# Kernel optimization log

Measured on AMD Instinct MI355X. Metric: run time of the kernel, lower is better.

Reference implementation:

```python
import jax, jax.numpy as jnp
import numpy as np
from jax import lax

EPS = 1e-5
TEM = 10.0  # self.tem at init; tem_proportion buffer is 0 so it stays 10.0


def _conv1d(x, w, padding, dilation=1, groups=1):
    # x: [B, C, S], w: [O, I//groups, K]
    return lax.conv_general_dilated(
        x, w, window_strides=(1,), padding=[(padding, padding)],
        rhs_dilation=(dilation,), dimension_numbers=('NCH', 'OIH', 'NCH'),
        feature_group_count=groups)


def _bn(y, gamma, beta):
    # training-mode BatchNorm1d: stats over (batch, length) per channel
    m = y.mean(axis=(0, 2), keepdims=True)
    v = y.var(axis=(0, 2), keepdims=True)
    return (y - m) * lax.rsqrt(v + EPS) * gamma[None, :, None] + beta[None, :, None]


def _nor_conv(x, w, g, b, k):
    return _bn(_conv1d(jax.nn.relu(x), w, padding=k // 2), g, b)


def _dil_conv(x, wd, wp, g, b, k):
    C = x.shape[1]
    y = _conv1d(jax.nn.relu(x), wd, padding=k - 1, dilation=2, groups=C)
    y = _conv1d(y, wp, padding=0)
    return _bn(y, g, b)


def _avg_pool3(x):
    s = lax.reduce_window(x, 0.0, lax.add, (1, 1, 3), (1, 1, 1),
                          [(0, 0), (0, 0), (1, 1)])
    return s / 3.0  # count_include_pad=True


def _max_pool3(x):
    return lax.reduce_window(x, -jnp.inf, lax.max, (1, 1, 3), (1, 1, 1),
                             [(0, 0), (0, 0), (1, 1)])


def _forward(x, u, arch_parameters,
             w_nor3, g_nor3, b_nor3, w_nor5, g_nor5, b_nor5,
             w_nor7, g_nor7, b_nor7,
             wd_dil3, wp_dil3, g_dil3, b_dil3,
             wd_dil5, wp_dil5, g_dil5, b_dil5,
             wd_dil7, wp_dil7, g_dil7, b_dil7):
    # ---- Gumbel straight-through gate (get_gumbel_prob) ----
    uc = jnp.clip(u, 1e-9, 1.0 - 1e-9)
    gumbels = -jnp.log(-jnp.log(uc))  # -log(Exp(1) sample)
    logits = (jax.nn.log_softmax(arch_parameters, axis=1) + gumbels) / TEM
    probs = jax.nn.softmax(logits, axis=1)          # [1, 10]
    index = jnp.argmax(probs, axis=-1)              # [1]
    one_h = jax.nn.one_hot(index, probs.shape[-1], dtype=probs.dtype)
    hardwts = one_h - lax.stop_gradient(probs) + probs  # straight-through

    # ---- forward_gdas: single edge (max_nodes=2) ----
    xc = jnp.transpose(x, (0, 2, 1))  # [B, H, S]: hidden=channels, seq=length
    branches = [
        lambda t: jnp.zeros_like(t),                         # none
        _avg_pool3,                                          # avg_pool_3
        _max_pool3,                                          # max_pool_3
        lambda t: _nor_conv(t, w_nor3, g_nor3, b_nor3, 3),   # nor_conv_3
        lambda t: _nor_conv(t, w_nor5, g_nor5, b_nor5, 5),   # nor_conv_5
        lambda t: _nor_conv(t, w_nor7, g_nor7, b_nor7, 7),   # nor_conv_7
        lambda t: _dil_conv(t, wd_dil3, wp_dil3, g_dil3, b_dil3, 3),
        lambda t: _dil_conv(t, wd_dil5, wp_dil5, g_dil5, b_dil5, 5),
        lambda t: _dil_conv(t, wd_dil7, wp_dil7, g_dil7, b_dil7, 7),
        lambda t: t,                                         # skip_connect
    ]
    idx = index[0]
    w = hardwts[0]                                  # [10]
    sel = lax.switch(idx, branches, xc)             # only argmax op is run
    w_sel = jnp.take(w, idx)
    # GDAS: w[argmax]*op(x) + sum of remaining scalar weights (broadcast add)
    out = w_sel * sel + (jnp.sum(w) - w_sel)
    out = jnp.transpose(out, (0, 2, 1))             # back to [B, S, H]
    return out + x                                  # residual


def setup_inputs() -> dict:
    key = jax.random.key(0)
    ks = jax.random.split(key, 16)
    B, S, H = 8, 512, 768
    d = {
        'x': jax.random.normal(ks[0], (B, S, H), jnp.float32),
        'u': jax.random.uniform(ks[1], (1, 10), jnp.float32),
        'arch_parameters': 0.001 * jax.random.normal(ks[2], (1, 10), jnp.float32),
    }
    i = 3
    for k in (3, 5, 7):
        d[f'w_nor{k}'] = 0.02 * jax.random.normal(ks[i], (H, H, k), jnp.float32); i += 1
        d[f'g_nor{k}'] = jnp.ones((H,), jnp.float32)
        d[f'b_nor{k}'] = jnp.zeros((H,), jnp.float32)
    for k in (3, 5, 7):
        d[f'wd_dil{k}'] = 0.1 * jax.random.normal(ks[i], (H, 1, k), jnp.float32); i += 1
        d[f'wp_dil{k}'] = 0.02 * jax.random.normal(ks[i], (H, H, 1), jnp.float32); i += 1
        d[f'g_dil{k}'] = jnp.ones((H,), jnp.float32)
        d[f'b_dil{k}'] = jnp.zeros((H,), jnp.float32)
    return d


def reference(x, u, arch_parameters,
              w_nor3, g_nor3, b_nor3, w_nor5, g_nor5, b_nor5,
              w_nor7, g_nor7, b_nor7,
              wd_dil3, wp_dil3, g_dil3, b_dil3,
              wd_dil5, wp_dil5, g_dil5, b_dil5,
              wd_dil7, wp_dil7, g_dil7, b_dil7):
    return _forward(x, u, arch_parameters,
                    w_nor3, g_nor3, b_nor3, w_nor5, g_nor5, b_nor5,
                    w_nor7, g_nor7, b_nor7,
                    wd_dil3, wp_dil3, g_dil3, b_dil3,
                    wd_dil5, wp_dil5, g_dil5, b_dil5,
                    wd_dil7, wp_dil7, g_dil7, b_dil7)
```

## Files before the change

### kernel.cpp

```cpp
#include <hip/hip_runtime.h>
#include <math.h>

#define BB 8
#define SS 512
#define HH 768
#define NTOT (BB*SS*HH)
#define EPSBN 1e-5f

typedef __attribute__((ext_vector_type(8))) short short8v;
typedef __attribute__((ext_vector_type(4))) float float4v;

struct Params {
  const float *x, *u, *ap;
  const float *w_nor3, *g_nor3, *b_nor3;
  const float *w_nor5, *g_nor5, *b_nor5;
  const float *w_nor7, *g_nor7, *b_nor7;
  const float *wd3, *wp3, *gd3, *bd3;
  const float *wd5, *wp5, *gd5, *bd5;
  const float *wd7, *wp7, *gd7, *bd7;
  float *out;
  float *hdr;
  float *y;
  float *z;
  float *psum;
  float *psq;
  float *mbuf;
  float *ibuf;
};

__device__ __forceinline__ short f2bf(float f) {
  union { float f; unsigned u; } v; v.f = f;
  unsigned r = v.u + 0x7FFF + ((v.u >> 16) & 1);
  return (short)(r >> 16);
}

__global__ void gate_kernel(Params p) {
  if (threadIdx.x != 0 || blockIdx.x != 0) return;
  float ap[10], lg[10], pr[10];
  float mx = -INFINITY;
  for (int i = 0; i < 10; i++) { ap[i] = p.ap[i]; mx = fmaxf(mx, ap[i]); }
  float se = 0.f;
  for (int i = 0; i < 10; i++) se += expf(ap[i] - mx);
  float lse = mx + logf(se);
  float lmax = -INFINITY;
  for (int i = 0; i < 10; i++) {
    float uc = fminf(fmaxf(p.u[i], 1e-9f), 1.f - 1e-9f);
    float gb = -logf(-logf(uc));
    lg[i] = ((ap[i] - lse) + gb) * 0.1f;
    lmax = fmaxf(lmax, lg[i]);
  }
  float ps = 0.f;
  for (int i = 0; i < 10; i++) { pr[i] = expf(lg[i] - lmax); ps += pr[i]; }
  int idx = 0; float best = -INFINITY;
  for (int i = 0; i < 10; i++) {
    pr[i] /= ps;
    if (pr[i] > best) { best = pr[i]; idx = i; }
  }
  float w_sel = (1.0f - pr[idx]) + pr[idx];
  p.hdr[0] = w_sel;
  p.hdr[1] = 0.0f;
  ((int*)p.hdr)[2] = idx;
}

__global__ __launch_bounds__(256) void dw_kernel(Params p) {
  int idx = ((const int*)p.hdr)[2];
  if (idx < 6 || idx > 8) return;
  int k = 3 + 2 * (idx - 6);
  const float* wd = (idx == 6) ? p.wd3 : (idx == 7) ? p.wd5 : p.wd7;
  int tid = blockIdx.x * 256 + threadIdx.x;
  if (tid >= NTOT) return;
  int c = tid % HH;
  int bs = tid / HH;
  int s = bs % SS;
  int b = bs / SS;
  float acc = 0.f;
  for (int dk = 0; dk < k; dk++) {
    int ss = s + 2 * dk - (k - 1);
    if (ss >= 0 && ss < SS) {
      float v = p.x[((size_t)(b * SS + ss)) * HH + c];
      acc += fmaxf(v, 0.f) * wd[c * k + dk];
    }
  }
  p.z[tid] = acc;
}

#define BM 128
#define BN 64
#define BK 32
#define LROW 40
__global__ __launch_bounds__(256) void conv_gemm_kernel(Params p) {
  int idx = ((const int*)p.hdr)[2];
  if (idx < 3 || idx > 8) return;
  bool nor = (idx <= 5);
  int k = nor ? (3 + 2 * (idx - 3)) : (3 + 2 * (idx - 6));
  const float* W = nor ? ((idx == 3) ? p.w_nor3 : (idx == 4) ? p.w_nor5 : p.w_nor7)
                       : ((idx == 6) ? p.wp3 : (idx == 7) ? p.wp5 : p.wp7);
  const float* A = nor ? p.x : p.z;
  int taps = nor ? k : 1;
  int halo = nor ? (k >> 1) : 0;

  __shared__ __attribute__((aligned(16))) short As[BM * LROW];
  __shared__ __attribute__((aligned(16))) short Bs[BN * LROW];

  int mt = blockIdx.x;
  int b = mt >> 2;
  int s0 = (mt & 3) * BM;
  int o0 = blockIdx.y * BN;

  int t = threadIdx.x;
  int lane = t & 63;
  int wid = t >> 6;
  int wm0 = (wid >> 1) * 64;
  int wn0 = (wid & 1) * 32;
  int l16 = lane & 15;
  int quad = lane >> 4;

  int sa_m = t >> 1;
  int sa_h = t & 1;
  int sb_n = t >> 2;
  int sb_seg = t & 3;

  float4v acc[4][2];
#pragma unroll
  for (int mi = 0; mi < 4; mi++)
#pragma unroll
    for (int ni = 0; ni < 2; ni++) acc[mi][ni] = (float4v){0.f, 0.f, 0.f, 0.f};

  for (int dk = 0; dk < taps; dk++) {
    int shift = dk - halo;
    for (int k0 = 0; k0 < HH; k0 += BK) {
      {
        int srow = s0 + sa_m + shift;
        float4 f[4];
        if (srow >= 0 && srow < SS) {
          const float* ap = A + ((size_t)(b * SS + srow)) * HH + k0 + sa_h * 16;
#pragma unroll
          for (int j = 0; j < 4; j++) f[j] = ((const float4*)ap)[j];
        } else {
#pragma unroll
          for (int j = 0; j < 4; j++) f[j] = (float4){0.f, 0.f, 0.f, 0.f};
        }
        short h16[16];
#pragma unroll
        for (int j = 0; j < 4; j++) {
          float vx = f[j].x, vy = f[j].y, vz = f[j].z, vw = f[j].w;
          if (nor) { vx = fmaxf(vx, 0.f); vy = fmaxf(vy, 0.f); vz = fmaxf(vz, 0.f); vw = fmaxf(vw, 0.f); }
          h16[4 * j + 0] = f2bf(vx); h16[4 * j + 1] = f2bf(vy);
          h16[4 * j + 2] = f2bf(vz); h16[4 * j + 3] = f2bf(vw);
        }
        short* dst = &As[sa_m * LROW + sa_h * 16];
        *(short8v*)dst = *(short8v*)&h16[0];
        *(short8v*)(dst + 8) = *(short8v*)&h16[8];
      }
      {
        short h8[8];
        int o = o0 + sb_n;
        if (!nor) {
          const float* bp = W + (size_t)o * HH + k0 + sb_seg * 8;
          float4 f0 = ((const float4*)bp)[0];
          float4 f1 = ((const float4*)bp)[1];
          h8[0] = f2bf(f0.x); h8[1] = f2bf(f0.y); h8[2] = f2bf(f0.z); h8[3] = f2bf(f0.w);
          h8[4] = f2bf(f1.x); h8[5] = f2bf(f1.y); h8[6] = f2bf(f1.z); h8[7] = f2bf(f1.w);
        } else {
#pragma unroll
          for (int j = 0; j < 8; j++) {
            int i = k0 + sb_seg * 8 + j;
            h8[j] = f2bf(W[((size_t)o * HH + i) * k + dk]);
          }
        }
        *(short8v*)&Bs[sb_n * LROW + sb_seg * 8] = *(short8v*)&h8[0];
      }
      __syncthreads();

      short8v af[4], bf[2];
#pragma unroll
      for (int mi = 0; mi < 4; mi++)
        af[mi] = *(const short8v*)&As[(wm0 + mi * 16 + l16) * LROW + quad * 8];
#pragma unroll
      for (int ni = 0; ni < 2; ni++)
        bf[ni] = *(const short8v*)&Bs[(wn0 + ni * 16 + l16) * LROW + quad * 8];
#pragma unroll
      for (int mi = 0; mi < 4; mi++)
#pragma unroll
        for (int ni = 0; ni < 2; ni++)
          acc[mi][ni] = __builtin_amdgcn_mfma_f32_16x16x32_bf16(af[mi], bf[ni], acc[mi][ni], 0, 0, 0);
      __syncthreads();
    }
  }

#pragma unroll
  for (int mi = 0; mi < 4; mi++) {
#pragma unroll
    for (int ni = 0; ni < 2; ni++) {
      int col = o0 + wn0 + ni * 16 + l16;
#pragma unroll
      for (int r = 0; r < 4; r++) {
        int row = s0 + wm0 + mi * 16 + quad * 4 + r;
        p.y[((size_t)(b * SS + row)) * HH + col] = acc[mi][ni][r];
      }
    }
  }
}

__global__ __launch_bounds__(256) void bn_stats1(Params p) {
  int idx = ((const int*)p.hdr)[2];
  if (idx < 3 || idx > 8) return;
  int t = threadIdx.x;
  int c = blockIdx.y * 64 + (t & 63);
  int rsub = t >> 6;
  float s = 0.f, q = 0.f;
  int rbase = blockIdx.x * 256 + rsub;
  for (int j = 0; j < 64; j++) {
    float v = p.y[(size_t)(rbase + 4 * j) * HH + c];
    s += v; q += v * v;
  }
  __shared__ float red[2][4][64];
  red[0][rsub][t & 63] = s;
  red[1][rsub][t & 63] = q;
  __syncthreads();
  if (t < 64) {
    float ts = red[0][0][t] + red[0][1][t] + red[0][2][t] + red[0][3][t];
    float tq = red[1][0][t] + red[1][1][t] + red[1][2][t] + red[1][3][t];
    p.psum[blockIdx.x * HH + blockIdx.y * 64 + t] = ts;
    p.psq[blockIdx.x * HH + blockIdx.y * 64 + t] = tq;
  }
}

__global__ __launch_bounds__(256) void bn_stats2(Params p) {
  int idx = ((const int*)p.hdr)[2];
  if (idx < 3 || idx > 8) return;
  int c = blockIdx.x * 256 + threadIdx.x;
  if (c >= HH) return;
  float s = 0.f, q = 0.f;
  for (int j = 0; j < 16; j++) { s += p.psum[j * HH + c]; q += p.psq[j * HH + c]; }
  float mean = s * (1.f / 4096.f);
  float var = q * (1.f / 4096.f) - mean * mean;
  p.mbuf[c] = mean;
  p.ibuf[c] = rsqrtf(var + EPSBN);
}

__global__ __launch_bounds__(256) void epilogue_kernel(Params p) {
  int idx = ((const int*)p.hdr)[2];
  float w_sel = p.hdr[0], w_rest = p.hdr[1];
  int tid = blockIdx.x * 256 + threadIdx.x;
  if (tid >= NTOT) return;
  float xv = p.x[tid];
  float sel;
  if (idx >= 3 && idx <= 8) {
    const float* g = (idx == 3) ? p.g_nor3 : (idx == 4) ? p.g_nor5 : (idx == 5) ? p.g_nor7
                   : (idx == 6) ? p.gd3 : (idx == 7) ? p.gd5 : p.gd7;
    const float* be = (idx == 3) ? p.b_nor3 : (idx == 4) ? p.b_nor5 : (idx == 5) ? p.b_nor7
                    : (idx == 6) ? p.bd3 : (idx == 7) ? p.bd5 : p.bd7;
    int h = tid % HH;
    float yv = p.y[tid];
    sel = (yv - p.mbuf[h]) * p.ibuf[h] * g[h] + be[h];
  } else if (idx == 0) {
    sel = 0.f;
  } else if (idx == 9) {
    sel = xv;
  } else {
    int bs = tid / HH;
    int s = bs % SS;
    if (idx == 1) {
      float xm = (s > 0) ? p.x[tid - HH] : 0.f;
      float xp = (s < SS - 1) ? p.x[tid + HH] : 0.f;
      sel = (xm + xv + xp) * (1.f / 3.f);
    } else {
      float xm = (s > 0) ? p.x[tid - HH] : -INFINITY;
      float xp = (s < SS - 1) ? p.x[tid + HH] : -INFINITY;
      sel = fmaxf(fmaxf(xm, xv), xp);
    }
  }
  p.out[tid] = w_sel * sel + w_rest + xv;
}

extern "C" void kernel_launch(void* const* d_in, const int* in_sizes, int n_in,
                              void* d_out, int out_size, void* d_ws, size_t ws_size,
                              hipStream_t stream) {
  Params p;
  p.x = (const float*)d_in[0];
  p.u = (const float*)d_in[1];
  p.ap = (const float*)d_in[2];
  p.w_nor3 = (const float*)d_in[3];  p.g_nor3 = (const float*)d_in[4];  p.b_nor3 = (const float*)d_in[5];
  p.w_nor5 = (const float*)d_in[6];  p.g_nor5 = (const float*)d_in[7];  p.b_nor5 = (const float*)d_in[8];
  p.w_nor7 = (const float*)d_in[9];  p.g_nor7 = (const float*)d_in[10]; p.b_nor7 = (const float*)d_in[11];
  p.wd3 = (const float*)d_in[12]; p.wp3 = (const float*)d_in[13]; p.gd3 = (const float*)d_in[14]; p.bd3 = (const float*)d_in[15];
  p.wd5 = (const float*)d_in[16]; p.wp5 = (const float*)d_in[17]; p.gd5 = (const float*)d_in[18]; p.bd5 = (const float*)d_in[19];
  p.wd7 = (const float*)d_in[20]; p.wp7 = (const float*)d_in[21]; p.gd7 = (const float*)d_in[22]; p.bd7 = (const float*)d_in[23];
  p.out = (float*)d_out;

  char* ws = (char*)d_ws;
  size_t off = 0;
  p.hdr = (float*)(ws + off); off += 256;
  p.y   = (float*)(ws + off); off += (size_t)NTOT * 4;
  p.z   = (float*)(ws + off); off += (size_t)NTOT * 4;
  p.psum = (float*)(ws + off); off += 16 * HH * 4;
  p.psq  = (float*)(ws + off); off += 16 * HH * 4;
  p.mbuf = (float*)(ws + off); off += HH * 4;
  p.ibuf = (float*)(ws + off); off += HH * 4;

  int nblk = (NTOT + 255) / 256;

  hipLaunchKernelGGL(gate_kernel, dim3(1), dim3(64), 0, stream, p);
  hipLaunchKernelGGL(dw_kernel, dim3(nblk), dim3(256), 0, stream, p);
  hipLaunchKernelGGL(conv_gemm_kernel, dim3(32, HH / BN), dim3(256), 0, stream, p);
  hipLaunchKernelGGL(bn_stats1, dim3(16, HH / 64), dim3(256), 0, stream, p);
  hipLaunchKernelGGL(bn_stats2, dim3((HH + 255) / 256), dim3(256), 0, stream, p);
  hipLaunchKernelGGL(epilogue_kernel, dim3(nblk), dim3(256), 0, stream, p);
}
```

Measured before the change: 145.1 us.

## Pre-convert activations and weights to bf16, use direct-to-LDS loads, fuse BN stats

```diff
diff --git a/kernel.cpp b/kernel.cpp
--- a/kernel.cpp
+++ b/kernel.cpp
@@ -6,6 +6,8 @@
 #define HH 768
 #define NTOT (BB*SS*HH)
 #define EPSBN 1e-5f
+#define SPAD 4
+#define SROWS (SS + 2*SPAD)
 
 typedef __attribute__((ext_vector_type(8))) short short8v;
 typedef __attribute__((ext_vector_type(4))) float float4v;
@@ -21,11 +23,10 @@
   float *out;
   float *hdr;
   float *y;
-  float *z;
+  short *xb;
+  short *wb;
   float *psum;
   float *psq;
-  float *mbuf;
-  float *ibuf;
 };
 
 __device__ __forceinline__ short f2bf(float f) {
@@ -35,7 +36,9 @@
 }
 
 __global__ void gate_kernel(Params p) {
-  if (threadIdx.x != 0 || blockIdx.x != 0) return;
+  int t = threadIdx.x;
+  for (int i = t; i < HH; i += 64) { p.psum[i] = 0.f; p.psq[i] = 0.f; }
+  if (t != 0) return;
   float ap[10], lg[10], pr[10];
   float mx = -INFINITY;
   for (int i = 0; i < 10; i++) { ap[i] = p.ap[i]; mx = fmaxf(mx, ap[i]); }
@@ -62,45 +65,96 @@
   ((int*)p.hdr)[2] = idx;
 }
 
-__global__ __launch_bounds__(256) void dw_kernel(Params p) {
+#define XBLK 1560
+#define WBLK 2016
+__global__ __launch_bounds__(256) void prep_kernel(Params p) {
   int idx = ((const int*)p.hdr)[2];
-  if (idx < 6 || idx > 8) return;
-  int k = 3 + 2 * (idx - 6);
-  const float* wd = (idx == 6) ? p.wd3 : (idx == 7) ? p.wd5 : p.wd7;
-  int tid = blockIdx.x * 256 + threadIdx.x;
-  if (tid >= NTOT) return;
-  int c = tid % HH;
-  int bs = tid / HH;
-  int s = bs % SS;
-  int b = bs / SS;
-  float acc = 0.f;
-  for (int dk = 0; dk < k; dk++) {
-    int ss = s + 2 * dk - (k - 1);
-    if (ss >= 0 && ss < SS) {
-      float v = p.x[((size_t)(b * SS + ss)) * HH + c];
-      acc += fmaxf(v, 0.f) * wd[c * k + dk];
-    }
-  }
-  p.z[tid] = acc;
+  if (idx < 3 || idx > 8) return;
+  int t = threadIdx.x;
+  if (blockIdx.x < XBLK) {
+    int u = blockIdx.x * 256 + t;
+    int c0 = (u % 96) * 8;
+    int row = (u / 96) % SROWS;
+    int b = u / (96 * SROWS);
+    int s = row - SPAD;
+    short8v o8 = (short8v){0,0,0,0,0,0,0,0};
+    if (s >= 0 && s < SS) {
+      float v[8];
+      if (idx <= 5) {
+        const float* xp = p.x + ((size_t)(b * SS + s) * HH + c0);
+        float4 f0 = ((const float4*)xp)[0];
+        float4 f1 = ((const float4*)xp)[1];
+        v[0] = fmaxf(f0.x, 0.f); v[1] = fmaxf(f0.y, 0.f);
+        v[2] = fmaxf(f0.z, 0.f); v[3] = fmaxf(f0.w, 0.f);
+        v[4] = fmaxf(f1.x, 0.f); v[5] = fmaxf(f1.y, 0.f);
+        v[6] = fmaxf(f1.z, 0.f); v[7] = fmaxf(f1.w, 0.f);
+      } else {
+        int k = 3 + 2 * (idx - 6);
+        const float* wd = (idx == 6) ? p.wd3 : (idx == 7) ? p.wd5 : p.wd7;
+#pragma unroll
+        for (int j = 0; j < 8; j++) v[j] = 0.f;
+        for (int dk = 0; dk < k; dk++) {
+          int ss = s + 2 * dk - (k - 1);
+          if (ss < 0 || ss >= SS) continue;
+          const float* xp = p.x + ((size_t)(b * SS + ss) * HH + c0);
+          float4 f0 = ((const float4*)xp)[0];
+          float4 f1 = ((const float4*)xp)[1];
+          float ff[8] = {f0.x, f0.y, f0.z, f0.w, f1.x, f1.y, f1.z, f1.w};
+#pragma unroll
+          for (int j = 0; j < 8; j++)
+            v[j] += fmaxf(ff[j], 0.f) * wd[(c0 + j) * k + dk];
+        }
+      }
+#pragma unroll
+      for (int j = 0; j < 8; j++) o8[j] = f2bf(v[j]);
+    }
+    *(short8v*)(p.xb + (size_t)(b * SROWS + row) * HH + c0) = o8;
+  } else {
+    int u = (blockIdx.x - XBLK) * 256 + t;
+    int i0 = (u % 96) * 8;
+    int o = (u / 96) % HH;
+    int dk = u / (96 * HH);
+    short8v o8;
+    if (idx <= 5) {
+      int k = 3 + 2 * (idx - 3);
+      if (dk >= k) return;
+      const float* W = (idx == 3) ? p.w_nor3 : (idx == 4) ? p.w_nor5 : p.w_nor7;
+#pragma unroll
+      for (int j = 0; j < 8; j++)
+        o8[j] = f2bf(W[((size_t)o * HH + i0 + j) * k + dk]);
+      *(short8v*)(p.wb + ((size_t)dk * HH + o) * HH + i0) = o8;
+    } else {
+      if (dk != 0) return;
+      const float* W = (idx == 6) ? p.wp3 : (idx == 7) ? p.wp5 : p.wp7;
+      const float* wp0 = W + (size_t)o * HH + i0;
+      float4 f0 = ((const float4*)wp0)[0];
+      float4 f1 = ((const float4*)wp0)[1];
+      o8[0] = f2bf(f0.x); o8[1] = f2bf(f0.y); o8[2] = f2bf(f0.z); o8[3] = f2bf(f0.w);
+      o8[4] = f2bf(f1.x); o8[5] = f2bf(f1.y); o8[6] = f2bf(f1.z); o8[7] = f2bf(f1.w);
+      *(short8v*)(p.wb + (size_t)o * HH + i0) = o8;
+    }
+  }
 }
 
 #define BM 128
 #define BN 64
-#define BK 32
-#define LROW 40
+#define BK 64
+
+typedef const __attribute__((address_space(1))) unsigned int* gas_t;
+typedef __attribute__((address_space(3))) unsigned int* las_t;
+__device__ __forceinline__ void gload16(const void* g, void* l) {
+  __builtin_amdgcn_global_load_lds((gas_t)g, (las_t)l, 16, 0, 0);
+}
+
 __global__ __launch_bounds__(256) void conv_gemm_kernel(Params p) {
   int idx = ((const int*)p.hdr)[2];
   if (idx < 3 || idx > 8) return;
   bool nor = (idx <= 5);
-  int k = nor ? (3 + 2 * (idx - 3)) : (3 + 2 * (idx - 6));
-  const float* W = nor ? ((idx == 3) ? p.w_nor3 : (idx == 4) ? p.w_nor5 : p.w_nor7)
-                       : ((idx == 6) ? p.wp3 : (idx == 7) ? p.wp5 : p.wp7);
-  const float* A = nor ? p.x : p.z;
-  int taps = nor ? k : 1;
-  int halo = nor ? (k >> 1) : 0;
-
-  __shared__ __attribute__((aligned(16))) short As[BM * LROW];
-  __shared__ __attribute__((aligned(16))) short Bs[BN * LROW];
+  int taps = nor ? (3 + 2 * (idx - 3)) : 1;
+  int halo = nor ? (taps >> 1) : 0;
+
+  __shared__ __attribute__((aligned(16))) short As[BM * BK];
+  __shared__ __attribute__((aligned(16))) short Bs[BN * BK];
 
   int mt = blockIdx.x;
   int b = mt >> 2;
@@ -109,87 +163,77 @@
 
   int t = threadIdx.x;
   int lane = t & 63;
-  int wid = t >> 6;
-  int wm0 = (wid >> 1) * 64;
-  int wn0 = (wid & 1) * 32;
-  int l16 = lane & 15;
-  int quad = lane >> 4;
-
-  int sa_m = t >> 1;
-  int sa_h = t & 1;
-  int sb_n = t >> 2;
-  int sb_seg = t & 3;
+  int w = t >> 6;
+  int l16 = lane & 15, quad = lane >> 4;
+  int wm0 = (w >> 1) * 64;
+  int wn0 = (w & 1) * 32;
+  int lr = lane >> 3;
+  int sw8 = ((lane & 7) ^ lr) * 8;
+
+  short* Al0 = &As[(32 * w) * BK];
+  short* Bl0 = &Bs[(16 * w) * BK];
 
   float4v acc[4][2];
 #pragma unroll
   for (int mi = 0; mi < 4; mi++)
 #pragma unroll
     for (int ni = 0; ni < 2; ni++) acc[mi][ni] = (float4v){0.f, 0.f, 0.f, 0.f};
+
+  const char* Ac = (const char*)As;
+  const char* Bc = (const char*)Bs;
+  int aro[4], bro[2], co[2];
+#pragma unroll
+  for (int mi = 0; mi < 4; mi++) aro[mi] = (wm0 + mi * 16 + l16) * (BK * 2);
+#pragma unroll
+  for (int ni = 0; ni < 2; ni++) bro[ni] = (wn0 + ni * 16 + l16) * (BK * 2);
+  int sx = (l16 & 7) << 4;
+  co[0] = (quad * 16) ^ sx;
+  co[1] = (64 + quad * 16) ^ sx;
 
   for (int dk = 0; dk < taps; dk++) {
     int shift = dk - halo;
+    const short* Ag[4]; const short* Bg[2];
+#pragma unroll
+    for (int j = 0; j < 4; j++) {
+      int tr = 32 * w + 8 * j + lr;
+      Ag[j] = p.xb + (size_t)(b * SROWS + SPAD + s0 + shift + tr) * HH + sw8;
+    }
+#pragma unroll
+    for (int j = 0; j < 2; j++) {
+      int tr = 16 * w + 8 * j + lr;
+      Bg[j] = p.wb + ((size_t)dk * HH + o0 + tr) * HH + sw8;
+    }
     for (int k0 = 0; k0 < HH; k0 += BK) {
-      {
-        int srow = s0 + sa_m + shift;
-        float4 f[4];
-        if (srow >= 0 && srow < SS) {
-          const float* ap = A + ((size_t)(b * SS + srow)) * HH + k0 + sa_h * 16;
-#pragma unroll
-          for (int j = 0; j < 4; j++) f[j] = ((const float4*)ap)[j];
-        } else {
-#pragma unroll
-          for (int j = 0; j < 4; j++) f[j] = (float4){0.f, 0.f, 0.f, 0.f};
-        }
-        short h16[16];
-#pragma unroll
-        for (int j = 0; j < 4; j++) {
-          float vx = f[j].x, vy = f[j].y, vz = f[j].z, vw = f[j].w;
-          if (nor) { vx = fmaxf(vx, 0.f); vy = fmaxf(vy, 0.f); vz = fmaxf(vz, 0.f); vw = fmaxf(vw, 0.f); }
-          h16[4 * j + 0] = f2bf(vx); h16[4 * j + 1] = f2bf(vy);
-          h16[4 * j + 2] = f2bf(vz); h16[4 * j + 3] = f2bf(vw);
-        }
-        short* dst = &As[sa_m * LROW + sa_h * 16];
-        *(short8v*)dst = *(short8v*)&h16[0];
-        *(short8v*)(dst + 8) = *(short8v*)&h16[8];
+#pragma unroll
+      for (int j = 0; j < 4; j++) gload16(Ag[j] + k0, Al0 + j * 8 * BK);
+#pragma unroll
+      for (int j = 0; j < 2; j++) gload16(Bg[j] + k0, Bl0 + j * 8 * BK);
+      __syncthreads();
+
+      short8v af[4][2], bf[2][2];
+#pragma unroll
+      for (int mi = 0; mi < 4; mi++) {
+        af[mi][0] = *(const short8v*)(Ac + aro[mi] + co[0]);
+        af[mi][1] = *(const short8v*)(Ac + aro[mi] + co[1]);
       }
-      {
-        short h8[8];
-        int o = o0 + sb_n;
-        if (!nor) {
-          const float* bp = W + (size_t)o * HH + k0 + sb_seg * 8;
-          float4 f0 = ((const float4*)bp)[0];
-          float4 f1 = ((const float4*)bp)[1];
-          h8[0] = f2bf(f0.x); h8[1] = f2bf(f0.y); h8[2] = f2bf(f0.z); h8[3] = f2bf(f0.w);
-          h8[4] = f2bf(f1.x); h8[5] = f2bf(f1.y); h8[6] = f2bf(f1.z); h8[7] = f2bf(f1.w);
-        } else {
-#pragma unroll
-          for (int j = 0; j < 8; j++) {
-            int i = k0 + sb_seg * 8 + j;
-            h8[j] = f2bf(W[((size_t)o * HH + i) * k + dk]);
-          }
-        }
-        *(short8v*)&Bs[sb_n * LROW + sb_seg * 8] = *(short8v*)&h8[0];
+#pragma unroll
+      for (int ni = 0; ni < 2; ni++) {
+        bf[ni][0] = *(const short8v*)(Bc + bro[ni] + co[0]);
+        bf[ni][1] = *(const short8v*)(Bc + bro[ni] + co[1]);
       }
+#pragma unroll
+      for (int h = 0; h < 2; h++)
+#pragma unroll
+        for (int mi = 0; mi < 4; mi++)
+#pragma unroll
+          for (int ni = 0; ni < 2; ni++)
+            acc[mi][ni] = __builtin_amdgcn_mfma_f32_16x16x32_bf16(af[mi][h], bf[ni][h], acc[mi][ni], 0, 0, 0);
       __syncthreads();
-
-      short8v af[4], bf[2];
-#pragma unroll
-      for (int mi = 0; mi < 4; mi++)
-        af[mi] = *(const short8v*)&As[(wm0 + mi * 16 + l16) * LROW + quad * 8];
-#pragma unroll
-      for (int ni = 0; ni < 2; ni++)
-        bf[ni] = *(const short8v*)&Bs[(wn0 + ni * 16 + l16) * LROW + quad * 8];
-#pragma unroll
-      for (int mi = 0; mi < 4; mi++)
-#pragma unroll
-        for (int ni = 0; ni < 2; ni++)
-          acc[mi][ni] = __builtin_amdgcn_mfma_f32_16x16x32_bf16(af[mi], bf[ni], acc[mi][ni], 0, 0, 0);
-      __syncthreads();
-    }
-  }
-
-#pragma unroll
-  for (int mi = 0; mi < 4; mi++) {
+    }
+  }
+
+#pragma unroll
+  for (int mi = 0; mi < 4; mi++)
 #pragma unroll
     for (int ni = 0; ni < 2; ni++) {
       int col = o0 + wn0 + ni * 16 + l16;
@@ -199,79 +243,82 @@
         p.y[((size_t)(b * SS + row)) * HH + col] = acc[mi][ni][r];
       }
     }
-  }
-}
-
-__global__ __launch_bounds__(256) void bn_stats1(Params p) {
-  int idx = ((const int*)p.hdr)[2];
-  if (idx < 3 || idx > 8) return;
-  int t = threadIdx.x;
-  int c = blockIdx.y * 64 + (t & 63);
-  int rsub = t >> 6;
-  float s = 0.f, q = 0.f;
-  int rbase = blockIdx.x * 256 + rsub;
-  for (int j = 0; j < 64; j++) {
-    float v = p.y[(size_t)(rbase + 4 * j) * HH + c];
-    s += v; q += v * v;
-  }
-  __shared__ float red[2][4][64];
-  red[0][rsub][t & 63] = s;
-  red[1][rsub][t & 63] = q;
-  __syncthreads();
-  if (t < 64) {
-    float ts = red[0][0][t] + red[0][1][t] + red[0][2][t] + red[0][3][t];
-    float tq = red[1][0][t] + red[1][1][t] + red[1][2][t] + red[1][3][t];
-    p.psum[blockIdx.x * HH + blockIdx.y * 64 + t] = ts;
-    p.psq[blockIdx.x * HH + blockIdx.y * 64 + t] = tq;
-  }
-}
-
-__global__ __launch_bounds__(256) void bn_stats2(Params p) {
-  int idx = ((const int*)p.hdr)[2];
-  if (idx < 3 || idx > 8) return;
-  int c = blockIdx.x * 256 + threadIdx.x;
-  if (c >= HH) return;
-  float s = 0.f, q = 0.f;
-  for (int j = 0; j < 16; j++) { s += p.psum[j * HH + c]; q += p.psq[j * HH + c]; }
-  float mean = s * (1.f / 4096.f);
-  float var = q * (1.f / 4096.f) - mean * mean;
-  p.mbuf[c] = mean;
-  p.ibuf[c] = rsqrtf(var + EPSBN);
+
+#pragma unroll
+  for (int ni = 0; ni < 2; ni++) {
+    float s = 0.f, q = 0.f;
+#pragma unroll
+    for (int mi = 0; mi < 4; mi++)
+#pragma unroll
+      for (int r = 0; r < 4; r++) { float v = acc[mi][ni][r]; s += v; q += v * v; }
+    s += __shfl_xor(s, 16); s += __shfl_xor(s, 32);
+    q += __shfl_xor(q, 16); q += __shfl_xor(q, 32);
+    if (lane < 16) {
+      int col = o0 + wn0 + ni * 16 + l16;
+      atomicAdd(&p.psum[col], s);
+      atomicAdd(&p.psq[col], q);
+    }
+  }
 }
 
 __global__ __launch_bounds__(256) void epilogue_kernel(Params p) {
   int idx = ((const int*)p.hdr)[2];
   float w_sel = p.hdr[0], w_rest = p.hdr[1];
-  int tid = blockIdx.x * 256 + threadIdx.x;
-  if (tid >= NTOT) return;
-  float xv = p.x[tid];
-  float sel;
+  int t4 = blockIdx.x * 256 + threadIdx.x;
+  int base = t4 * 4;
+  float4 xv = *(const float4*)(p.x + base);
+  float4 sel;
   if (idx >= 3 && idx <= 8) {
     const float* g = (idx == 3) ? p.g_nor3 : (idx == 4) ? p.g_nor5 : (idx == 5) ? p.g_nor7
                    : (idx == 6) ? p.gd3 : (idx == 7) ? p.gd5 : p.gd7;
     const float* be = (idx == 3) ? p.b_nor3 : (idx == 4) ? p.b_nor5 : (idx == 5) ? p.b_nor7
                     : (idx == 6) ? p.bd3 : (idx == 7) ? p.bd5 : p.bd7;
-    int h = tid % HH;
-    float yv = p.y[tid];
-    sel = (yv - p.mbuf[h]) * p.ibuf[h] * g[h] + be[h];
+    int c = base % HH;
+    float4 yv = *(const float4*)(p.y + base);
+    float4 ps = *(const float4*)(p.psum + c);
+    float4 pq = *(const float4*)(p.psq + c);
+    float4 gv = *(const float4*)(g + c);
+    float4 bv = *(const float4*)(be + c);
+    const float inv = 1.f / 4096.f;
+    float m0 = ps.x * inv, m1 = ps.y * inv, m2 = ps.z * inv, m3 = ps.w * inv;
+    float i0 = rsqrtf(pq.x * inv - m0 * m0 + EPSBN);
+    float i1 = rsqrtf(pq.y * inv - m1 * m1 + EPSBN);
+    float i2 = rsqrtf(pq.z * inv - m2 * m2 + EPSBN);
+    float i3 = rsqrtf(pq.w * inv - m3 * m3 + EPSBN);
+    sel.x = (yv.x - m0) * i0 * gv.x + bv.x;
+    sel.y = (yv.y - m1) * i1 * gv.y + bv.y;
+    sel.z = (yv.z - m2) * i2 * gv.z + bv.z;
+    sel.w = (yv.w - m3) * i3 * gv.w + bv.w;
   } else if (idx == 0) {
-    sel = 0.f;
+    sel = (float4){0.f, 0.f, 0.f, 0.f};
   } else if (idx == 9) {
     sel = xv;
   } else {
-    int bs = tid / HH;
-    int s = bs % SS;
+    int s = (base / HH) % SS;
+    float4 xm, xp;
     if (idx == 1) {
-      float xm = (s > 0) ? p.x[tid - HH] : 0.f;
-      float xp = (s < SS - 1) ? p.x[tid + HH] : 0.f;
-      sel = (xm + xv + xp) * (1.f / 3.f);
+      xm = (s > 0)      ? *(const float4*)(p.x + base - HH) : (float4){0.f, 0.f, 0.f, 0.f};
+      xp = (s < SS - 1) ? *(const float4*)(p.x + base + HH) : (float4){0.f, 0.f, 0.f, 0.f};
+      const float th = 1.f / 3.f;
+      sel.x = (xm.x + xv.x + xp.x) * th;
+      sel.y = (xm.y + xv.y + xp.y) * th;
+      sel.z = (xm.z + xv.z + xp.z) * th;
+      sel.w = (xm.w + xv.w + xp.w) * th;
     } else {
-      float xm = (s > 0) ? p.x[tid - HH] : -INFINITY;
-      float xp = (s < SS - 1) ? p.x[tid + HH] : -INFINITY;
-      sel = fmaxf(fmaxf(xm, xv), xp);
-    }
-  }
-  p.out[tid] = w_sel * sel + w_rest + xv;
+      xm = (s > 0)      ? *(const float4*)(p.x + base - HH) : (float4){-INFINITY, -INFINITY, -INFINITY, -INFINITY};
+      xp = (s < SS - 1) ? *(const float4*)(p.x + base + HH) : (float4){-INFINITY, -INFINITY, -INFINITY, -INFINITY};
+      sel.x = fmaxf(fmaxf(xm.x, xv.x), xp.x);
+      sel.y = fmaxf(fmaxf(xm.y, xv.y), xp.y);
+      sel.z = fmaxf(fmaxf(xm.z, xv.z), xp.z);
+      sel.w = fmaxf(fmaxf(xm.w, xv.w), xp.w);
+    }
+  }
+  float4 ov;
+  ov.x = w_sel * sel.x + w_rest + xv.x;
+  ov.y = w_sel * sel.y + w_rest + xv.y;
+  ov.z = w_sel * sel.z + w_rest + xv.z;
+  ov.w = w_sel * sel.w + w_rest + xv.w;
+  *(float4*)(p.out + base) = ov;
 }
 
 extern "C" void kernel_launch(void* const* d_in, const int* in_sizes, int n_in,
@@ -293,18 +340,13 @@
   size_t off = 0;
   p.hdr = (float*)(ws + off); off += 256;
   p.y   = (float*)(ws + off); off += (size_t)NTOT * 4;
-  p.z   = (float*)(ws + off); off += (size_t)NTOT * 4;
-  p.psum = (float*)(ws + off); off += 16 * HH * 4;
-  p.psq  = (float*)(ws + off); off += 16 * HH * 4;
-  p.mbuf = (float*)(ws + off); off += HH * 4;
-  p.ibuf = (float*)(ws + off); off += HH * 4;
-
-  int nblk = (NTOT + 255) / 256;
+  p.xb  = (short*)(ws + off); off += (size_t)BB * SROWS * HH * 2;
+  p.wb  = (short*)(ws + off); off += (size_t)7 * HH * HH * 2;
+  p.psum = (float*)(ws + off); off += HH * 4;
+  p.psq  = (float*)(ws + off); off += HH * 4;
 
   hipLaunchKernelGGL(gate_kernel, dim3(1), dim3(64), 0, stream, p);
-  hipLaunchKernelGGL(dw_kernel, dim3(nblk), dim3(256), 0, stream, p);
-  hipLaunchKernelGGL(conv_gemm_kernel, dim3(32, HH / BN), dim3(256), 0, stream, p);
-  hipLaunchKernelGGL(bn_stats1, dim3(16, HH / 64), dim3(256), 0, stream, p);
-  hipLaunchKernelGGL(bn_stats2, dim3((HH + 255) / 256), dim3(256), 0, stream, p);
-  hipLaunchKernelGGL(epilogue_kernel, dim3(nblk), dim3(256), 0, stream, p);
-}
+  hipLaunchKernelGGL(prep_kernel, dim3(XBLK + WBLK), dim3(256), 0, stream, p);
+  hipLaunchKernelGGL(conv_gemm_kernel, dim3(SS * BB / BM, HH / BN), dim3(256), 0, stream, p);
+  hipLaunchKernelGGL(epilogue_kernel, dim3(NTOT / 4 / 256), dim3(256), 0, stream, p);
+}
```

New measurement: 137.0 us. 1.06x faster.
